# Kernel tuning notes

Hardware: AMD Instinct MI355X
Metric: run time of the kernel (lower is better)

The kernel has to match this reference:

```python
import jax, jax.numpy as jnp
import numpy as np

LN_EPS = 1e-5
NORM_EPS = 1e-12


def channel_layernorm(x, w, b):
    # LayerNorm over channel dim of NCHW tensor (torch permutes to NHWC; equivalent)
    mu = x.mean(axis=1, keepdims=True)
    var = x.var(axis=1, keepdims=True)
    xn = (x - mu) / jnp.sqrt(var + LN_EPS)
    return xn * w[None, :, None, None] + b[None, :, None, None]


def pconv(x, w):
    # 1x1 pointwise conv, w: (out_ch, in_ch)
    return jnp.einsum('bchw,oc->bohw', x, w)


def dwconv3(x, w):
    # depthwise 3x3, padding 1; w: (ch, 1, 3, 3)
    return jax.lax.conv_general_dilated(
        x, w, window_strides=(1, 1), padding='SAME',
        feature_group_count=x.shape[1],
        dimension_numbers=('NCHW', 'OIHW', 'NCHW'))


def l2norm(x):
    n = jnp.sqrt(jnp.sum(x * x, axis=-1, keepdims=True))
    return x / jnp.maximum(n, NORM_EPS)


def setup_inputs() -> dict:
    key = jax.random.key(0)
    ks = jax.random.split(key, 8)
    B, C, H, W = 4, 128, 128, 128
    NH, G = 8, 2

    def w(k, shape, fan_in):
        return jax.random.normal(k, shape, dtype=jnp.float32) * (fan_in ** -0.5)

    return {
        'x': jax.random.normal(ks[0], (B, C, H, W), dtype=jnp.float32),
        'ln1_w': jnp.ones((C,), jnp.float32),
        'ln1_b': jnp.zeros((C,), jnp.float32),
        'temperature': jnp.ones((NH, 1, 1), jnp.float32),
        'qkv_p_w': w(ks[1], (3 * C, C), C),
        'qkv_d_w': w(ks[2], (3 * C, 1, 3, 3), 9),
        'proj_w': w(ks[3], (C, C), C),
        'ln2_w': jnp.ones((C,), jnp.float32),
        'ln2_b': jnp.zeros((C,), jnp.float32),
        'g1_w': w(ks[4], (2 * G * C, C), C),
        'gd_w': w(ks[5], (2 * G * C, 1, 3, 3), 9),
        'g2_w': w(ks[6], (C, G * C), G * C),
        'num_heads': NH,
    }


def reference(x, ln1_w, ln1_b, temperature, qkv_p_w, qkv_d_w, proj_w,
              ln2_w, ln2_b, g1_w, gd_w, g2_w, num_heads):
    b, c, h, w_ = x.shape
    d = c // num_heads

    # --- MDTA branch ---
    y = channel_layernorm(x, ln1_w, ln1_b)
    qkv = dwconv3(pconv(y, qkv_p_w), qkv_d_w)  # (b, 3c, h, w)
    q, k, v = jnp.split(qkv, 3, axis=1)
    q = l2norm(q.reshape(b, num_heads, d, h * w_))
    k = l2norm(k.reshape(b, num_heads, d, h * w_))
    v = v.reshape(b, num_heads, d, h * w_)
    # transposed (channel) attention: (b, heads, d, d)
    attn = jnp.einsum('bhdn,bhen->bhde', q, k) * temperature[None]
    attn = jax.nn.softmax(attn, axis=-1)
    out = jnp.einsum('bhde,bhen->bhdn', attn, v).reshape(b, c, h, w_)
    x = x + pconv(out, proj_w)

    # --- GDFN branch ---
    y = channel_layernorm(x, ln2_w, ln2_b)
    hdn = dwconv3(pconv(y, g1_w), gd_w)  # (b, 2*gamma*c, h, w)
    x1, x2 = jnp.split(hdn, 2, axis=1)
    g = jax.nn.gelu(x1, approximate=False) * x2
    x = x + pconv(g, g2_w)
    return x
```

## Files before the change

### kernel.cpp

```cpp
#include <hip/hip_runtime.h>
#include <cstdint>
#include <cstddef>

typedef float f32x4 __attribute__((ext_vector_type(4)));
typedef __bf16 bf16x8 __attribute__((ext_vector_type(8)));

__device__ __forceinline__ float b2f(unsigned short u) {
    union { unsigned int i; float f; } z; z.i = ((unsigned int)u) << 16; return z.f;
}
__device__ __forceinline__ unsigned short f2b(float f) {
    union { float f; unsigned int i; } z; z.f = f;
    unsigned int x = z.i;
    return (unsigned short)((x + 0x7FFFu + ((x >> 16) & 1u)) >> 16);
}

static constexpr int C = 128;
static constexpr int NP = 16384;
static constexpr int NH = 8;

struct Ptr11 { const float* p[11]; };
__constant__ int kWN[11]   = {128, 128, 8, 49152, 3456, 16384, 128, 128, 65536, 4608, 32768};
__constant__ int kWOff[11] = {0, 128, 256, 272, 49424, 52880, 69264, 69392, 69520, 135056, 139664};
static constexpr int kWTotal = 172432;

__global__ __launch_bounds__(256)
void cvt_w_kernel(Ptr11 P, unsigned short* __restrict__ dst)
{
    int seg = blockIdx.y;
    int n = kWN[seg];
    int i = blockIdx.x * 256 + threadIdx.x;
    if (i >= n) return;
    dst[kWOff[seg] + i] = f2b(P.p[seg][i]);
}

template <int COUT>
__device__ __forceinline__ void gemm_core_tr(
    const unsigned short* BsT,
    const unsigned short* __restrict__ W,
    unsigned short* __restrict__ OutB,
    int n0, int tid)
{
    const int lane = tid & 63;
    const int wid  = tid >> 6;
    const int ln16 = lane & 15, quad = lane >> 4;
    const int wy = wid >> 1, wx = wid & 1;
    const char* bs = (const char*)BsT;
    const int swz = (ln16 & 7) << 4;
    int rbase[4];
    #pragma unroll
    for (int nt = 0; nt < 4; ++nt) {
        int n = wx * 64 + nt * 16 + ln16;
        rbase[nt] = n * 256 + quad * 16;
    }

    for (int cc = 0; cc < COUT / 128; ++cc) {
        const int m0 = cc * 128;
        f32x4 acc[4][4];
        #pragma unroll
        for (int i = 0; i < 4; ++i)
            #pragma unroll
            for (int j = 0; j < 4; ++j) acc[i][j] = f32x4{0.f, 0.f, 0.f, 0.f};

        #pragma unroll
        for (int k0 = 0; k0 < 128; k0 += 32) {
            bf16x8 afr[4], bfr[4];
            #pragma unroll
            for (int mt = 0; mt < 4; ++mt) {
                int m = m0 + wy * 64 + mt * 16 + ln16;
                uint4 v = *(const uint4*)(W + (size_t)m * 128 + k0 + quad * 8);
                afr[mt] = *(bf16x8*)&v;
            }
            #pragma unroll
            for (int nt = 0; nt < 4; ++nt) {
                uint4 v = *(const uint4*)(bs + ((rbase[nt] + k0 * 2) ^ swz));
                bfr[nt] = *(bf16x8*)&v;
            }
            #pragma unroll
            for (int mt = 0; mt < 4; ++mt)
                #pragma unroll
                for (int nt = 0; nt < 4; ++nt)
                    acc[mt][nt] = __builtin_amdgcn_mfma_f32_16x16x32_bf16(
                        afr[mt], bfr[nt], acc[mt][nt], 0, 0, 0);
        }
        #pragma unroll
        for (int mt = 0; mt < 4; ++mt)
            #pragma unroll
            for (int nt = 0; nt < 4; ++nt) {
                int co0 = m0 + wy * 64 + mt * 16 + quad * 4;
                int n = n0 + wx * 64 + nt * 16 + ln16;
                #pragma unroll
                for (int r = 0; r < 4; ++r)
                    OutB[(size_t)(co0 + r) * NP + n] = f2b(acc[mt][nt][r]);
            }
    }
}

template <int COUT>
__global__ __launch_bounds__(256)
void lngemm_kernel(const float* __restrict__ x,
                   const unsigned short* __restrict__ lg,
                   const unsigned short* __restrict__ lb,
                   const unsigned short* __restrict__ W,
                   unsigned short* __restrict__ Out)
{
    __shared__ unsigned short BsT[128 * 128];
    __shared__ float Ssum[8][128], Ssq[8][128], Mu[128], Rs[128];
    const int tid = threadIdx.x;
    const int b = blockIdx.y;
    const int n0 = blockIdx.x * 128;
    const int pxg = tid & 31;
    const int cseg = tid >> 5;
    const float* xb = x + (size_t)b * C * NP + n0 + pxg * 4;

    f32x4 hv[16];
    f32x4 vs = f32x4{0.f, 0.f, 0.f, 0.f}, vq = f32x4{0.f, 0.f, 0.f, 0.f};
    #pragma unroll
    for (int i = 0; i < 16; ++i) {
        f32x4 v = *(const f32x4*)(xb + (size_t)(cseg * 16 + i) * NP);
        hv[i] = v; vs += v; vq += v * v;
    }
    #pragma unroll
    for (int j = 0; j < 4; ++j) {
        Ssum[cseg][pxg * 4 + j] = vs[j];
        Ssq[cseg][pxg * 4 + j]  = vq[j];
    }
    __syncthreads();
    if (tid < 128) {
        float s = 0.f, q = 0.f;
        #pragma unroll
        for (int e = 0; e < 8; ++e) { s += Ssum[e][tid]; q += Ssq[e][tid]; }
        float mu = s * (1.f / 128.f);
        float var = q * (1.f / 128.f) - mu * mu;
        Mu[tid] = mu;
        Rs[tid] = rsqrtf(fmaxf(var, 0.f) + 1e-5f);
    }
    __syncthreads();
    f32x4 mu4 = *(const f32x4*)(&Mu[pxg * 4]);
    f32x4 rs4 = *(const f32x4*)(&Rs[pxg * 4]);

    float gwv[16], bwv[16];
    #pragma unroll
    for (int i = 0; i < 16; ++i) {
        gwv[i] = b2f(lg[cseg * 16 + i]);
        bwv[i] = b2f(lb[cseg * 16 + i]);
    }

    char* p = (char*)BsT;
    #pragma unroll
    for (int j = 0; j < 4; ++j) {
        int n = pxg * 4 + j;
        union { uint4 v[2]; unsigned short u[16]; } o;
        #pragma unroll
        for (int i = 0; i < 16; ++i)
            o.u[i] = f2b((hv[i][j] - mu4[j]) * rs4[j] * gwv[i] + bwv[i]);
        int base = n * 256 + cseg * 32;
        int sw = (n & 7) << 4;
        *(uint4*)(p + (base ^ sw))        = o.v[0];
        *(uint4*)(p + ((base + 16) ^ sw)) = o.v[1];
    }
    __syncthreads();
    gemm_core_tr<COUT>(BsT, W, Out + (size_t)b * COUT * NP, n0, tid);
}

template <int COUT>
__global__ __launch_bounds__(256)
void gemm_bf16t_kernel(const unsigned short* __restrict__ W,
                       const unsigned short* __restrict__ Xt,
                       unsigned short* __restrict__ Out)
{
    __shared__ unsigned short BsT[128 * 128];
    const int tid = threadIdx.x;
    const int b = blockIdx.y;
    const int n0 = blockIdx.x * 128;
    const unsigned short* Xb = Xt + (size_t)b * NP * 128 + (size_t)n0 * 128;
    char* p = (char*)BsT;
    #pragma unroll
    for (int r = 0; r < 8; ++r) {
        int flat = tid + r * 256;
        int n = flat >> 4, ks = flat & 15;
        uint4 v = *(const uint4*)(Xb + (size_t)n * 128 + ks * 8);
        *(uint4*)(p + ((n * 256 + ks * 16) ^ ((n & 7) << 4))) = v;
    }
    __syncthreads();
    gemm_core_tr<COUT>(BsT, W, Out + (size_t)b * COUT * NP, n0, tid);
}

__global__ __launch_bounds__(256)
void projln_kernel(const unsigned short* __restrict__ W,
                   const unsigned short* __restrict__ Yt,
                   const float* __restrict__ Res,
                   float* __restrict__ Xmid,
                   const unsigned short* __restrict__ lg,
                   const unsigned short* __restrict__ lb,
                   unsigned short* __restrict__ Y2t)
{
    __shared__ unsigned short BsT[128 * 128];
    __shared__ float RedS[2][128], RedQ[2][128], Mu[128], Rs[128];
    const int tid = threadIdx.x;
    const int b = blockIdx.y;
    const int n0 = blockIdx.x * 128;
    char* p = (char*)BsT;
    {
        const unsigned short* Xb = Yt + (size_t)b * NP * 128 + (size_t)n0 * 128;
        #pragma unroll
        for (int r = 0; r < 8; ++r) {
            int flat = tid + r * 256;
            int n = flat >> 4, ks = flat & 15;
            uint4 v = *(const uint4*)(Xb + (size_t)n * 128 + ks * 8);
            *(uint4*)(p + ((n * 256 + ks * 16) ^ ((n & 7) << 4))) = v;
        }
    }
    __syncthreads();

    const int lane = tid & 63, wid = tid >> 6;
    const int ln16 = lane & 15, quad = lane >> 4;
    const int wy = wid >> 1, wx = wid & 1;
    const int swz = (ln16 & 7) << 4;
    int rbase[4];
    #pragma unroll
    for (int nt = 0; nt < 4; ++nt) {
        int n = wx * 64 + nt * 16 + ln16;
        rbase[nt] = n * 256 + quad * 16;
    }

    f32x4 acc[4][4];
    #pragma unroll
    for (int i = 0; i < 4; ++i)
        #pragma unroll
        for (int j = 0; j < 4; ++j) acc[i][j] = f32x4{0.f, 0.f, 0.f, 0.f};

    #pragma unroll
    for (int k0 = 0; k0 < 128; k0 += 32) {
        bf16x8 afr[4], bfr[4];
        #pragma unroll
        for (int mt = 0; mt < 4; ++mt) {
            int m = wy * 64 + mt * 16 + ln16;
            uint4 v = *(const uint4*)(W + (size_t)m * 128 + k0 + quad * 8);
            afr[mt] = *(bf16x8*)&v;
        }
        #pragma unroll
        for (int nt = 0; nt < 4; ++nt) {
            uint4 v = *(const uint4*)(p + ((rbase[nt] + k0 * 2) ^ swz));
            bfr[nt] = *(bf16x8*)&v;
        }
        #pragma unroll
        for (int mt = 0; mt < 4; ++mt)
            #pragma unroll
            for (int nt = 0; nt < 4; ++nt)
                acc[mt][nt] = __builtin_amdgcn_mfma_f32_16x16x32_bf16(
                    afr[mt], bfr[nt], acc[mt][nt], 0, 0, 0);
    }

    size_t base = (size_t)b * 128 * NP;
    float ps[4] = {0.f, 0.f, 0.f, 0.f}, pq[4] = {0.f, 0.f, 0.f, 0.f};
    #pragma unroll
    for (int mt = 0; mt < 4; ++mt)
        #pragma unroll
        for (int nt = 0; nt < 4; ++nt) {
            int co0 = wy * 64 + mt * 16 + quad * 4;
            int n = n0 + wx * 64 + nt * 16 + ln16;
            #pragma unroll
            for (int r = 0; r < 4; ++r) {
                size_t idx = base + (size_t)(co0 + r) * NP + n;
                float t = Res[idx] + acc[mt][nt][r];
                Xmid[idx] = t;
                acc[mt][nt][r] = t;
                ps[nt] += t; pq[nt] += t * t;
            }
        }
    #pragma unroll
    for (int nt = 0; nt < 4; ++nt) {
        ps[nt] += __shfl_xor(ps[nt], 16, 64); ps[nt] += __shfl_xor(ps[nt], 32, 64);
        pq[nt] += __shfl_xor(pq[nt], 16, 64); pq[nt] += __shfl_xor(pq[nt], 32, 64);
    }
    if (quad == 0) {
        #pragma unroll
        for (int nt = 0; nt < 4; ++nt) {
            int nn = wx * 64 + nt * 16 + ln16;
            RedS[wy][nn] = ps[nt]; RedQ[wy][nn] = pq[nt];
        }
    }
    __syncthreads();
    if (tid < 128) {
        float s = RedS[0][tid] + RedS[1][tid];
        float q = RedQ[0][tid] + RedQ[1][tid];
        float mu = s * (1.f / 128.f);
        float var = q * (1.f / 128.f) - mu * mu;
        Mu[tid] = mu; Rs[tid] = rsqrtf(fmaxf(var, 0.f) + 1e-5f);
    }
    __syncthreads();

    #pragma unroll
    for (int mt = 0; mt < 4; ++mt) {
        int co0 = wy * 64 + mt * 16 + quad * 4;
        union { uint2 v; unsigned short u[4]; } gv, bv;
        gv.v = *(const uint2*)(lg + co0);
        bv.v = *(const uint2*)(lb + co0);
        float gw[4], bw[4];
        #pragma unroll
        for (int r = 0; r < 4; ++r) { gw[r] = b2f(gv.u[r]); bw[r] = b2f(bv.u[r]); }
        #pragma unroll
        for (int nt = 0; nt < 4; ++nt) {
            int nn = wx * 64 + nt * 16 + ln16;
            float mu = Mu[nn], rs = Rs[nn];
            union { uint2 v; unsigned short u[4]; } t2;
            #pragma unroll
            for (int r = 0; r < 4; ++r)
                t2.u[r] = f2b((acc[mt][nt][r] - mu) * rs * gw[r] + bw[r]);
            int addr = (nn * 256 + co0 * 2) ^ ((nn & 7) << 4);
            *(uint2*)(p + addr) = t2.v;
        }
    }
    __syncthreads();

    unsigned short* Yo = Y2t + (size_t)b * NP * 128 + (size_t)n0 * 128;
    #pragma unroll
    for (int r = 0; r < 8; ++r) {
        int flat = tid + r * 256;
        int n = flat >> 4, ks = flat & 15;
        uint4 v = *(const uint4*)(p + ((n * 256 + ks * 16) ^ ((n & 7) << 4)));
        *(uint4*)(Yo + (size_t)n * 128 + ks * 8) = v;
    }
}

template <int K, int EPI>
__global__ __launch_bounds__(256)
void gemm_pconv(const unsigned short* __restrict__ W,
                const unsigned short* __restrict__ X,
                void* __restrict__ Out,
                const float* __restrict__ Res,
                int Cout)
{
    __shared__ unsigned short Bs[32][130];
    const int tid = threadIdx.x;
    const int b = blockIdx.z;
    const int n0 = blockIdx.x * 128;
    const int m0 = blockIdx.y * 128;
    const unsigned short* Xb = X + (size_t)b * K * NP;
    const int wid = tid >> 6;
    const int lane = tid & 63;
    const int ln16 = lane & 15;
    const int quad = lane >> 4;
    const int wy = wid >> 1;
    const int wx = wid & 1;

    f32x4 acc[4][4];
    #pragma unroll
    for (int i = 0; i < 4; ++i)
        #pragma unroll
        for (int j = 0; j < 4; ++j)
            acc[i][j] = f32x4{0.f, 0.f, 0.f, 0.f};

    for (int k0 = 0; k0 < K; k0 += 32) {
        #pragma unroll
        for (int r = 0; r < 2; ++r) {
            int flat = tid + r * 256;
            int kk = flat >> 4;
            int nn = (flat & 15) * 8;
            uint4 v = *(const uint4*)(Xb + (size_t)(k0 + kk) * NP + n0 + nn);
            unsigned int* d = (unsigned int*)&Bs[kk][nn];
            d[0] = v.x; d[1] = v.y; d[2] = v.z; d[3] = v.w;
        }
        __syncthreads();

        bf16x8 afr[4];
        #pragma unroll
        for (int mt = 0; mt < 4; ++mt) {
            int m = m0 + wy * 64 + mt * 16 + ln16;
            uint4 v = *(const uint4*)(W + (size_t)m * K + k0 + quad * 8);
            afr[mt] = *(bf16x8*)&v;
        }
        bf16x8 bfr[4];
        #pragma unroll
        for (int nt = 0; nt < 4; ++nt) {
            int n = wx * 64 + nt * 16 + ln16;
            union { bf16x8 v; unsigned short u[8]; } tmp;
            #pragma unroll
            for (int j = 0; j < 8; ++j) tmp.u[j] = Bs[quad * 8 + j][n];
            bfr[nt] = tmp.v;
        }
        #pragma unroll
        for (int mt = 0; mt < 4; ++mt)
            #pragma unroll
            for (int nt = 0; nt < 4; ++nt)
                acc[mt][nt] = __builtin_amdgcn_mfma_f32_16x16x32_bf16(
                    afr[mt], bfr[nt], acc[mt][nt], 0, 0, 0);
        __syncthreads();
    }

    size_t outbase = (size_t)b * Cout * NP;
    #pragma unroll
    for (int mt = 0; mt < 4; ++mt) {
        #pragma unroll
        for (int nt = 0; nt < 4; ++nt) {
            int co0 = m0 + wy * 64 + mt * 16 + quad * 4;
            int n = n0 + wx * 64 + nt * 16 + ln16;
            #pragma unroll
            for (int r = 0; r < 4; ++r) {
                float v = acc[mt][nt][r];
                size_t idx = outbase + (size_t)(co0 + r) * NP + n;
                if (EPI == 0) ((unsigned short*)Out)[idx] = f2b(v);
                else          ((float*)Out)[idx] = Res[idx] + v;
            }
        }
    }
}

__global__ __launch_bounds__(256)
void dwconv3_kernel(const unsigned short* __restrict__ in,
                    const unsigned short* __restrict__ w9,
                    unsigned short* __restrict__ out, int CH)
{
    int t = blockIdx.x * 256 + threadIdx.x;
    int xi = (t & 15) * 8;
    int y  = (t >> 4) & 127;
    int bc = t >> 11;
    int c  = bc % CH;
    const unsigned short* base = in + (size_t)bc * NP + y * 128 + xi;

    float wr[9];
    #pragma unroll
    for (int i = 0; i < 9; ++i) wr[i] = b2f(w9[c * 9 + i]);

    uint4 rv0 = uint4{0,0,0,0}, rv1, rv2 = uint4{0,0,0,0};
    if (y > 0)   rv0 = *(const uint4*)(base - 128);
    rv1 = *(const uint4*)(base);
    if (y < 127) rv2 = *(const uint4*)(base + 128);
    uint4 rows[3] = {rv0, rv1, rv2};

    float o[8];
    #pragma unroll
    for (int j = 0; j < 8; ++j) o[j] = 0.f;

    #pragma unroll
    for (int r = 0; r < 3; ++r) {
        union { uint4 v; unsigned short u[8]; } cv; cv.v = rows[r];
        int lh = __shfl_up((int)cv.u[7], 1, 16);
        int rh = __shfl_down((int)cv.u[0], 1, 16);
        float p[10];
        p[0] = (xi > 0)   ? b2f((unsigned short)lh) : 0.f;
        p[9] = (xi < 120) ? b2f((unsigned short)rh) : 0.f;
        #pragma unroll
        for (int j = 0; j < 8; ++j) p[j + 1] = b2f(cv.u[j]);
        #pragma unroll
        for (int j = 0; j < 8; ++j)
            o[j] += wr[r * 3] * p[j] + wr[r * 3 + 1] * p[j + 1] + wr[r * 3 + 2] * p[j + 2];
    }
    union { uint4 v; unsigned short u[8]; } res;
    #pragma unroll
    for (int j = 0; j < 8; ++j) res.u[j] = f2b(o[j]);
    *(uint4*)(out + (size_t)bc * NP + y * 128 + xi) = res.v;
}

__global__ __launch_bounds__(256)
void dwgelu_kernel(const unsigned short* __restrict__ hdn,
                   const unsigned short* __restrict__ w9,
                   unsigned short* __restrict__ g)
{
    int t = blockIdx.x * 256 + threadIdx.x;
    int xi = (t & 15) * 8;
    int y  = (t >> 4) & 127;
    int bc = t >> 11;
    int c  = bc & 255;
    int b  = bc >> 8;
    const unsigned short* base1 = hdn + ((size_t)b * 512 + c) * NP + y * 128 + xi;
    const unsigned short* base2 = base1 + (size_t)256 * NP;

    float w1[9], w2[9];
    #pragma unroll
    for (int i = 0; i < 9; ++i) {
        w1[i] = b2f(w9[c * 9 + i]);
        w2[i] = b2f(w9[(c + 256) * 9 + i]);
    }

    uint4 ra0 = uint4{0,0,0,0}, ra1, ra2 = uint4{0,0,0,0};
    uint4 rb0 = uint4{0,0,0,0}, rb1, rb2 = uint4{0,0,0,0};
    if (y > 0)   { ra0 = *(const uint4*)(base1 - 128); rb0 = *(const uint4*)(base2 - 128); }
    ra1 = *(const uint4*)(base1);
    rb1 = *(const uint4*)(base2);
    if (y < 127) { ra2 = *(const uint4*)(base1 + 128); rb2 = *(const uint4*)(base2 + 128); }
    uint4 rowsA[3] = {ra0, ra1, ra2};
    uint4 rowsB[3] = {rb0, rb1, rb2};

    float a1[8], a2[8];
    #pragma unroll
    for (int j = 0; j < 8; ++j) { a1[j] = 0.f; a2[j] = 0.f; }

    #pragma unroll
    for (int r = 0; r < 3; ++r) {
        union { uint4 v; unsigned short u[8]; } c1, c2;
        c1.v = rowsA[r]; c2.v = rowsB[r];
        int lh1 = __shfl_up((int)c1.u[7], 1, 16);
        int rh1 = __shfl_down((int)c1.u[0], 1, 16);
        int lh2 = __shfl_up((int)c2.u[7], 1, 16);
        int rh2 = __shfl_down((int)c2.u[0], 1, 16);
        float p1[10], p2[10];
        p1[0] = (xi > 0)   ? b2f((unsigned short)lh1) : 0.f;
        p1[9] = (xi < 120) ? b2f((unsigned short)rh1) : 0.f;
        p2[0] = (xi > 0)   ? b2f((unsigned short)lh2) : 0.f;
        p2[9] = (xi < 120) ? b2f((unsigned short)rh2) : 0.f;
        #pragma unroll
        for (int j = 0; j < 8; ++j) { p1[j + 1] = b2f(c1.u[j]); p2[j + 1] = b2f(c2.u[j]); }
        #pragma unroll
        for (int j = 0; j < 8; ++j) {
            a1[j] += w1[r * 3] * p1[j] + w1[r * 3 + 1] * p1[j + 1] + w1[r * 3 + 2] * p1[j + 2];
            a2[j] += w2[r * 3] * p2[j] + w2[r * 3 + 1] * p2[j + 1] + w2[r * 3 + 2] * p2[j + 2];
        }
    }
    union { uint4 v; unsigned short u[8]; } res;
    #pragma unroll
    for (int j = 0; j < 8; ++j) {
        float u = a1[j];
        float tt = u * (0.7978845608f + 0.0356774081f * u * u);
        float e = __expf(2.f * tt);
        float th = 1.f - 2.f / (e + 1.f);
        float ge = 0.5f * u * (1.f + th);
        res.u[j] = f2b(ge * a2[j]);
    }
    *(uint4*)(g + (size_t)bc * NP + y * 128 + xi) = res.v;
}

__global__ __launch_bounds__(256)
void gramss_kernel(const unsigned short* __restrict__ qkv,
                   float* __restrict__ Spart, float* __restrict__ Npart)
{
    int h = blockIdx.x, b = blockIdx.y, sp = blockIdx.z;
    int wid = threadIdx.x >> 6, lane = threadIdx.x & 63;
    int ln16 = lane & 15, quad = lane >> 4;
    int nbase = sp * 2048 + wid * 512;
    const unsigned short* qp = qkv + ((size_t)b * 384 + h * 16 + ln16) * NP;
    const unsigned short* kp = qkv + ((size_t)b * 384 + 128 + h * 16 + ln16) * NP;
    f32x4 acc = f32x4{0.f, 0.f, 0.f, 0.f};
    float qs = 0.f, ks = 0.f;
    for (int i = 0; i < 512; i += 32) {
        int n = nbase + i + quad * 8;
        uint4 av = *(const uint4*)(qp + n);
        uint4 bv = *(const uint4*)(kp + n);
        union { uint4 v; unsigned short u[8]; } ua, ub;
        ua.v = av; ub.v = bv;
        #pragma unroll
        for (int j = 0; j < 8; ++j) {
            float qv = b2f(ua.u[j]); qs += qv * qv;
            float kv = b2f(ub.u[j]); ks += kv * kv;
        }
        acc = __builtin_amdgcn_mfma_f32_16x16x32_bf16(*(bf16x8*)&av, *(bf16x8*)&bv, acc, 0, 0, 0);
    }
    int bh = b * NH + h;
    float* Sp = Spart + ((size_t)bh * 32 + sp * 4 + wid) * 256;
    #pragma unroll
    for (int r = 0; r < 4; ++r)
        Sp[(quad * 4 + r) * 16 + ln16] = acc[r];

    qs += __shfl_xor(qs, 16, 64); qs += __shfl_xor(qs, 32, 64);
    ks += __shfl_xor(ks, 16, 64); ks += __shfl_xor(ks, 32, 64);
    __shared__ float G[4][32];
    if (quad == 0) { G[wid][ln16] = qs; G[wid][16 + ln16] = ks; }
    __syncthreads();
    if (threadIdx.x < 32) {
        float s = G[0][threadIdx.x] + G[1][threadIdx.x] + G[2][threadIdx.x] + G[3][threadIdx.x];
        Npart[((size_t)bh * 8 + sp) * 32 + threadIdx.x] = s;
    }
}

__global__ __launch_bounds__(256)
void softmax2_kernel(const float* __restrict__ Spart, const float* __restrict__ Npart,
                     const unsigned short* __restrict__ temp, float* __restrict__ P)
{
    int bh = blockIdx.x;
    int h = bh & 7;
    int t = threadIdx.x;
    int dq = t >> 4, dk = t & 15;
    float sacc = 0.f;
    const float* Sp = Spart + (size_t)bh * 32 * 256;
    #pragma unroll
    for (int j = 0; j < 32; ++j) sacc += Sp[j * 256 + t];
    const float* Np = Npart + (size_t)bh * 8 * 32;
    float sq = 0.f, sk = 0.f;
    #pragma unroll
    for (int sp = 0; sp < 8; ++sp) { sq += Np[sp * 32 + dq]; sk += Np[sp * 32 + 16 + dk]; }
    float nq = fmaxf(sqrtf(sq), 1e-12f);
    float nk = fmaxf(sqrtf(sk), 1e-12f);
    float v = sacc / (nq * nk) * b2f(temp[h]);
    float m = v;
    #pragma unroll
    for (int o = 8; o > 0; o >>= 1) m = fmaxf(m, __shfl_xor(m, o, 16));
    float e = __expf(v - m);
    float s = e;
    #pragma unroll
    for (int o = 8; o > 0; o >>= 1) s += __shfl_xor(s, o, 16);
    P[(size_t)bh * 256 + t] = e / s;
}

__global__ __launch_bounds__(256)
void attnv_kernel(const float* __restrict__ P, const unsigned short* __restrict__ qkv,
                  unsigned short* __restrict__ yt)
{
    __shared__ float Ps[256];
    int h = blockIdx.y, b = blockIdx.z;
    Ps[threadIdx.x] = P[((size_t)b * NH + h) * 256 + threadIdx.x];
    __syncthreads();
    int n = (blockIdx.x * 256 + threadIdx.x) * 4;
    const unsigned short* vp = qkv + ((size_t)b * 384 + 256 + h * 16) * NP + n;
    float o[16][4];
    #pragma unroll
    for (int d = 0; d < 16; ++d)
        #pragma unroll
        for (int j = 0; j < 4; ++j) o[d][j] = 0.f;
    #pragma unroll
    for (int e = 0; e < 16; ++e) {
        union { uint2 v; unsigned short u[4]; } cv;
        cv.v = *(const uint2*)(vp + (size_t)e * NP);
        float v0 = b2f(cv.u[0]), v1 = b2f(cv.u[1]), v2 = b2f(cv.u[2]), v3 = b2f(cv.u[3]);
        #pragma unroll
        for (int d = 0; d < 16; ++d) {
            float p = Ps[d * 16 + e];
            o[d][0] += p * v0; o[d][1] += p * v1; o[d][2] += p * v2; o[d][3] += p * v3;
        }
    }
    unsigned short* op = yt + (size_t)b * NP * C + (size_t)n * C + h * 16;
    #pragma unroll
    for (int j = 0; j < 4; ++j) {
        union { uint4 v; unsigned short u[8]; } r1, r2;
        #pragma unroll
        for (int d = 0; d < 8; ++d) r1.u[d] = f2b(o[d][j]);
        #pragma unroll
        for (int d = 0; d < 8; ++d) r2.u[d] = f2b(o[8 + d][j]);
        *(uint4*)(op + (size_t)j * C)     = r1.v;
        *(uint4*)(op + (size_t)j * C + 8) = r2.v;
    }
}

struct Bufs {
    float* xmid;
    unsigned short* y;
    unsigned short* y2;
    unsigned short* big;
    unsigned short* mid;
    float* Spart;
    float* P;
    float* Npart;
};

static void run_pipeline(const float* x_f32, float* out_f32,
                         const unsigned short* w,
                         const Bufs& B, int nb, hipStream_t stream)
{
    const unsigned short* ln1_w   = w + 0;
    const unsigned short* ln1_b   = w + 128;
    const unsigned short* temp    = w + 256;
    const unsigned short* qkv_p_w = w + 272;
    const unsigned short* qkv_d_w = w + 49424;
    const unsigned short* proj_w  = w + 52880;
    const unsigned short* ln2_w   = w + 69264;
    const unsigned short* ln2_b   = w + 69392;
    const unsigned short* g1_w    = w + 69520;
    const unsigned short* gd_w    = w + 135056;
    const unsigned short* g2_w    = w + 139664;

    lngemm_kernel<384><<<dim3(NP / 128, nb), 256, 0, stream>>>(x_f32, ln1_w, ln1_b, qkv_p_w, B.big);
    dwconv3_kernel<<<nb * 384 * NP / 2048, 256, 0, stream>>>(B.big, qkv_d_w, B.mid, 384);
    gramss_kernel<<<dim3(NH, nb, 8), 256, 0, stream>>>(B.mid, B.Spart, B.Npart);
    softmax2_kernel<<<nb * NH, 256, 0, stream>>>(B.Spart, B.Npart, temp, B.P);
    attnv_kernel<<<dim3(NP / 1024, NH, nb), 256, 0, stream>>>(B.P, B.mid, B.y);
    projln_kernel<<<dim3(NP / 128, nb), 256, 0, stream>>>(proj_w, B.y, x_f32, B.xmid, ln2_w, ln2_b, B.y2);

    gemm_bf16t_kernel<512><<<dim3(NP / 128, nb), 256, 0, stream>>>(g1_w, B.y2, B.big);
    dwgelu_kernel<<<nb * 256 * NP / 2048, 256, 0, stream>>>(B.big, gd_w, B.mid);
    gemm_pconv<256, 1><<<dim3(NP / 128, 1, nb), 256, 0, stream>>>(g2_w, B.mid, out_f32, B.xmid, 128);
}

extern "C" void kernel_launch(void* const* d_in, const int* in_sizes, int n_in,
                              void* d_out, int out_size, void* d_ws, size_t ws_size,
                              hipStream_t stream)
{
    (void)in_sizes; (void)n_in; (void)out_size;
    const float* x = (const float*)d_in[0];
    char* ws = (char*)d_ws;

    size_t off = 0;
    unsigned short* wpack = (unsigned short*)(ws + off);
    off += (size_t)kWTotal * 2;
    off = (off + 255) & ~(size_t)255;
    size_t header = off;

    auto layout = [&](int nb, size_t o, Bufs& B) -> size_t {
        B.xmid = (float*)(ws + o);           o += (size_t)nb * C * NP * 4;
        B.y    = (unsigned short*)(ws + o);  o += (size_t)nb * C * NP * 2;
        B.y2   = (unsigned short*)(ws + o);  o += (size_t)nb * C * NP * 2;
        B.big  = (unsigned short*)(ws + o);  o += (size_t)nb * 512 * NP * 2;
        B.mid  = (unsigned short*)(ws + o);  o += (size_t)nb * 384 * NP * 2;
        B.Spart = (float*)(ws + o);          o += (size_t)nb * NH * 32 * 256 * 4;
        B.P     = (float*)(ws + o);          o += (size_t)nb * NH * 256 * 4;
        B.Npart = (float*)(ws + o);          o += (size_t)nb * NH * 8 * 32 * 4;
        return o;
    };

    Ptr11 P;
    for (int i = 0; i < 11; ++i) P.p[i] = (const float*)d_in[i + 1];
    cvt_w_kernel<<<dim3(256, 11), 256, 0, stream>>>(P, wpack);

    Bufs Bfull;
    size_t need_full = layout(4, header, Bfull);

    if (ws_size >= need_full) {
        run_pipeline(x, (float*)d_out, wpack, Bfull, 4, stream);
    } else {
        Bufs B1;
        layout(1, header, B1);
        for (int b = 0; b < 4; ++b) {
            run_pipeline(x + (size_t)b * C * NP,
                         (float*)d_out + (size_t)b * C * NP,
                         wpack, B1, 1, stream);
        }
    }
}
```

Measured before the change: 266.7 us.

## Fuse QKV depthwise conv into Gram and attention-V kernels, drop qkv intermediate

The separate depthwise 3x3 conv over the 384 qkv channels is removed. The q/k depthwise conv is now computed inside a new Gram kernel, which stages 4-row tiles in LDS, computes sum-of-squares partials and reduces the per-wave MFMA partials in shared memory. The v depthwise conv is recomputed on the fly inside the attention-V kernel. This avoids writing and re-reading the full bf16 qkv intermediate and saves one launch, at the cost of extra halo loads, redundant row reads, and more partial sums (32 splits) for the softmax kernel to reduce.

```diff
diff --git a/kernel.cpp b/kernel.cpp
--- a/kernel.cpp
+++ b/kernel.cpp
@@ -31,6 +31,32 @@
     int i = blockIdx.x * 256 + threadIdx.x;
     if (i >= n) return;
     dst[kWOff[seg] + i] = f2b(P.p[seg][i]);
+}
+
+__device__ __forceinline__ void dw8(const unsigned short* base, int y, int xi,
+                                    const float* wr, float* o)
+{
+    uint4 rv0 = uint4{0,0,0,0}, rv1, rv2 = uint4{0,0,0,0};
+    if (y > 0)   rv0 = *(const uint4*)(base - 128);
+    rv1 = *(const uint4*)(base);
+    if (y < 127) rv2 = *(const uint4*)(base + 128);
+    uint4 rows[3] = {rv0, rv1, rv2};
+    #pragma unroll
+    for (int j = 0; j < 8; ++j) o[j] = 0.f;
+    #pragma unroll
+    for (int r = 0; r < 3; ++r) {
+        union { uint4 v; unsigned short u[8]; } cv; cv.v = rows[r];
+        int lh = __shfl_up((int)cv.u[7], 1, 16);
+        int rh = __shfl_down((int)cv.u[0], 1, 16);
+        float p[10];
+        p[0] = (xi > 0)   ? b2f((unsigned short)lh) : 0.f;
+        p[9] = (xi < 120) ? b2f((unsigned short)rh) : 0.f;
+        #pragma unroll
+        for (int j = 0; j < 8; ++j) p[j + 1] = b2f(cv.u[j]);
+        #pragma unroll
+        for (int j = 0; j < 8; ++j)
+            o[j] += wr[r * 3] * p[j] + wr[r * 3 + 1] * p[j + 1] + wr[r * 3 + 2] * p[j + 2];
+    }
 }
 
 template <int COUT>
@@ -407,52 +433,6 @@
 }
 
 __global__ __launch_bounds__(256)
-void dwconv3_kernel(const unsigned short* __restrict__ in,
-                    const unsigned short* __restrict__ w9,
-                    unsigned short* __restrict__ out, int CH)
-{
-    int t = blockIdx.x * 256 + threadIdx.x;
-    int xi = (t & 15) * 8;
-    int y  = (t >> 4) & 127;
-    int bc = t >> 11;
-    int c  = bc % CH;
-    const unsigned short* base = in + (size_t)bc * NP + y * 128 + xi;
-
-    float wr[9];
-    #pragma unroll
-    for (int i = 0; i < 9; ++i) wr[i] = b2f(w9[c * 9 + i]);
-
-    uint4 rv0 = uint4{0,0,0,0}, rv1, rv2 = uint4{0,0,0,0};
-    if (y > 0)   rv0 = *(const uint4*)(base - 128);
-    rv1 = *(const uint4*)(base);
-    if (y < 127) rv2 = *(const uint4*)(base + 128);
-    uint4 rows[3] = {rv0, rv1, rv2};
-
-    float o[8];
-    #pragma unroll
-    for (int j = 0; j < 8; ++j) o[j] = 0.f;
-
-    #pragma unroll
-    for (int r = 0; r < 3; ++r) {
-        union { uint4 v; unsigned short u[8]; } cv; cv.v = rows[r];
-        int lh = __shfl_up((int)cv.u[7], 1, 16);
-        int rh = __shfl_down((int)cv.u[0], 1, 16);
-        float p[10];
-        p[0] = (xi > 0)   ? b2f((unsigned short)lh) : 0.f;
-        p[9] = (xi < 120) ? b2f((unsigned short)rh) : 0.f;
-        #pragma unroll
-        for (int j = 0; j < 8; ++j) p[j + 1] = b2f(cv.u[j]);
-        #pragma unroll
-        for (int j = 0; j < 8; ++j)
-            o[j] += wr[r * 3] * p[j] + wr[r * 3 + 1] * p[j + 1] + wr[r * 3 + 2] * p[j + 2];
-    }
-    union { uint4 v; unsigned short u[8]; } res;
-    #pragma unroll
-    for (int j = 0; j < 8; ++j) res.u[j] = f2b(o[j]);
-    *(uint4*)(out + (size_t)bc * NP + y * 128 + xi) = res.v;
-}
-
-__global__ __launch_bounds__(256)
 void dwgelu_kernel(const unsigned short* __restrict__ hdn,
                    const unsigned short* __restrict__ w9,
                    unsigned short* __restrict__ g)
@@ -473,40 +453,10 @@
         w2[i] = b2f(w9[(c + 256) * 9 + i]);
     }
 
-    uint4 ra0 = uint4{0,0,0,0}, ra1, ra2 = uint4{0,0,0,0};
-    uint4 rb0 = uint4{0,0,0,0}, rb1, rb2 = uint4{0,0,0,0};
-    if (y > 0)   { ra0 = *(const uint4*)(base1 - 128); rb0 = *(const uint4*)(base2 - 128); }
-    ra1 = *(const uint4*)(base1);
-    rb1 = *(const uint4*)(base2);
-    if (y < 127) { ra2 = *(const uint4*)(base1 + 128); rb2 = *(const uint4*)(base2 + 128); }
-    uint4 rowsA[3] = {ra0, ra1, ra2};
-    uint4 rowsB[3] = {rb0, rb1, rb2};
-
     float a1[8], a2[8];
-    #pragma unroll
-    for (int j = 0; j < 8; ++j) { a1[j] = 0.f; a2[j] = 0.f; }
-
-    #pragma unroll
-    for (int r = 0; r < 3; ++r) {
-        union { uint4 v; unsigned short u[8]; } c1, c2;
-        c1.v = rowsA[r]; c2.v = rowsB[r];
-        int lh1 = __shfl_up((int)c1.u[7], 1, 16);
-        int rh1 = __shfl_down((int)c1.u[0], 1, 16);
-        int lh2 = __shfl_up((int)c2.u[7], 1, 16);
-        int rh2 = __shfl_down((int)c2.u[0], 1, 16);
-        float p1[10], p2[10];
-        p1[0] = (xi > 0)   ? b2f((unsigned short)lh1) : 0.f;
-        p1[9] = (xi < 120) ? b2f((unsigned short)rh1) : 0.f;
-        p2[0] = (xi > 0)   ? b2f((unsigned short)lh2) : 0.f;
-        p2[9] = (xi < 120) ? b2f((unsigned short)rh2) : 0.f;
-        #pragma unroll
-        for (int j = 0; j < 8; ++j) { p1[j + 1] = b2f(c1.u[j]); p2[j + 1] = b2f(c2.u[j]); }
-        #pragma unroll
-        for (int j = 0; j < 8; ++j) {
-            a1[j] += w1[r * 3] * p1[j] + w1[r * 3 + 1] * p1[j + 1] + w1[r * 3 + 2] * p1[j + 2];
-            a2[j] += w2[r * 3] * p2[j] + w2[r * 3 + 1] * p2[j + 1] + w2[r * 3 + 2] * p2[j + 2];
-        }
-    }
+    dw8(base1, y, xi, w1, a1);
+    dw8(base2, y, xi, w2, a2);
+
     union { uint4 v; unsigned short u[8]; } res;
     #pragma unroll
     for (int j = 0; j < 8; ++j) {
@@ -521,45 +471,66 @@
 }
 
 __global__ __launch_bounds__(256)
-void gramss_kernel(const unsigned short* __restrict__ qkv,
-                   float* __restrict__ Spart, float* __restrict__ Npart)
-{
-    int h = blockIdx.x, b = blockIdx.y, sp = blockIdx.z;
-    int wid = threadIdx.x >> 6, lane = threadIdx.x & 63;
-    int ln16 = lane & 15, quad = lane >> 4;
-    int nbase = sp * 2048 + wid * 512;
-    const unsigned short* qp = qkv + ((size_t)b * 384 + h * 16 + ln16) * NP;
-    const unsigned short* kp = qkv + ((size_t)b * 384 + 128 + h * 16 + ln16) * NP;
+void dwqkgram_kernel(const unsigned short* __restrict__ big,
+                     const unsigned short* __restrict__ w9,
+                     float* __restrict__ Spart,
+                     float* __restrict__ Npart)
+{
+    __shared__ unsigned short qs_[16 * 520];
+    __shared__ unsigned short ks_[16 * 520];
+    __shared__ float Sred[4][256];
+    const int h = blockIdx.x, b = blockIdx.y, sp = blockIdx.z;
+    const int tid = threadIdx.x;
+    const int wid = tid >> 6, lane = tid & 63;
+    const int xi = (tid & 15) * 8;
+    const int yr = (tid >> 4) & 3;
+    const int y  = sp * 4 + yr;
+    const int bh = b * NH + h;
+    float* Np = Npart + ((size_t)bh * 32 + sp) * 32;
+
+    #pragma unroll
+    for (int p = 0; p < 4; ++p) {
+        int qc = p * 4 + wid;
+        #pragma unroll
+        for (int s = 0; s < 2; ++s) {
+            int ch = s * 128 + h * 16 + qc;
+            const unsigned short* base = big + ((size_t)b * 384 + ch) * NP + y * 128 + xi;
+            float wr[9];
+            #pragma unroll
+            for (int i = 0; i < 9; ++i) wr[i] = b2f(w9[ch * 9 + i]);
+            float o[8];
+            dw8(base, y, xi, wr, o);
+            union { uint4 v; unsigned short u[8]; } res;
+            float ss = 0.f;
+            #pragma unroll
+            for (int j = 0; j < 8; ++j) {
+                res.u[j] = f2b(o[j]);
+                float vv = b2f(res.u[j]);
+                ss += vv * vv;
+            }
+            unsigned short* tile = s ? ks_ : qs_;
+            *(uint4*)(&tile[qc * 520 + yr * 128 + xi]) = res.v;
+            #pragma unroll
+            for (int od = 32; od > 0; od >>= 1) ss += __shfl_xor(ss, od, 64);
+            if (lane == 0) Np[s * 16 + qc] = ss;
+        }
+    }
+    __syncthreads();
+
+    const int ln16 = lane & 15, quad = lane >> 4;
     f32x4 acc = f32x4{0.f, 0.f, 0.f, 0.f};
-    float qs = 0.f, ks = 0.f;
-    for (int i = 0; i < 512; i += 32) {
-        int n = nbase + i + quad * 8;
-        uint4 av = *(const uint4*)(qp + n);
-        uint4 bv = *(const uint4*)(kp + n);
-        union { uint4 v; unsigned short u[8]; } ua, ub;
-        ua.v = av; ub.v = bv;
-        #pragma unroll
-        for (int j = 0; j < 8; ++j) {
-            float qv = b2f(ua.u[j]); qs += qv * qv;
-            float kv = b2f(ub.u[j]); ks += kv * kv;
-        }
-        acc = __builtin_amdgcn_mfma_f32_16x16x32_bf16(*(bf16x8*)&av, *(bf16x8*)&bv, acc, 0, 0, 0);
-    }
-    int bh = b * NH + h;
-    float* Sp = Spart + ((size_t)bh * 32 + sp * 4 + wid) * 256;
-    #pragma unroll
-    for (int r = 0; r < 4; ++r)
-        Sp[(quad * 4 + r) * 16 + ln16] = acc[r];
-
-    qs += __shfl_xor(qs, 16, 64); qs += __shfl_xor(qs, 32, 64);
-    ks += __shfl_xor(ks, 16, 64); ks += __shfl_xor(ks, 32, 64);
-    __shared__ float G[4][32];
-    if (quad == 0) { G[wid][ln16] = qs; G[wid][16 + ln16] = ks; }
-    __syncthreads();
-    if (threadIdx.x < 32) {
-        float s = G[0][threadIdx.x] + G[1][threadIdx.x] + G[2][threadIdx.x] + G[3][threadIdx.x];
-        Npart[((size_t)bh * 8 + sp) * 32 + threadIdx.x] = s;
-    }
+    #pragma unroll
+    for (int i = 0; i < 4; ++i) {
+        int off = wid * 128 + i * 32 + quad * 8;
+        uint4 qv = *(const uint4*)(&qs_[ln16 * 520 + off]);
+        uint4 kv = *(const uint4*)(&ks_[ln16 * 520 + off]);
+        acc = __builtin_amdgcn_mfma_f32_16x16x32_bf16(*(bf16x8*)&qv, *(bf16x8*)&kv, acc, 0, 0, 0);
+    }
+    #pragma unroll
+    for (int r = 0; r < 4; ++r) Sred[wid][(quad * 4 + r) * 16 + ln16] = acc[r];
+    __syncthreads();
+    float ssum = Sred[0][tid] + Sred[1][tid] + Sred[2][tid] + Sred[3][tid];
+    Spart[((size_t)bh * 32 + sp) * 256 + tid] = ssum;
 }
 
 __global__ __launch_bounds__(256)
@@ -574,10 +545,10 @@
     const float* Sp = Spart + (size_t)bh * 32 * 256;
     #pragma unroll
     for (int j = 0; j < 32; ++j) sacc += Sp[j * 256 + t];
-    const float* Np = Npart + (size_t)bh * 8 * 32;
+    const float* Np = Npart + (size_t)bh * 32 * 32;
     float sq = 0.f, sk = 0.f;
     #pragma unroll
-    for (int sp = 0; sp < 8; ++sp) { sq += Np[sp * 32 + dq]; sk += Np[sp * 32 + 16 + dk]; }
+    for (int sp = 0; sp < 32; ++sp) { sq += Np[sp * 32 + dq]; sk += Np[sp * 32 + 16 + dk]; }
     float nq = fmaxf(sqrtf(sq), 1e-12f);
     float nk = fmaxf(sqrtf(sk), 1e-12f);
     float v = sacc / (nq * nk) * b2f(temp[h]);
@@ -592,31 +563,60 @@
 }
 
 __global__ __launch_bounds__(256)
-void attnv_kernel(const float* __restrict__ P, const unsigned short* __restrict__ qkv,
-                  unsigned short* __restrict__ yt)
+void attnvdw_kernel(const float* __restrict__ P, const unsigned short* __restrict__ big,
+                    const unsigned short* __restrict__ w9,
+                    unsigned short* __restrict__ yt)
 {
     __shared__ float Ps[256];
     int h = blockIdx.y, b = blockIdx.z;
     Ps[threadIdx.x] = P[((size_t)b * NH + h) * 256 + threadIdx.x];
     __syncthreads();
-    int n = (blockIdx.x * 256 + threadIdx.x) * 4;
-    const unsigned short* vp = qkv + ((size_t)b * 384 + 256 + h * 16) * NP + n;
+    int t = threadIdx.x;
+    int n = (blockIdx.x * 256 + t) * 4;
+    int y  = n >> 7;
+    int x0 = n & 127;
+
     float o[16][4];
     #pragma unroll
     for (int d = 0; d < 16; ++d)
         #pragma unroll
         for (int j = 0; j < 4; ++j) o[d][j] = 0.f;
+
     #pragma unroll
     for (int e = 0; e < 16; ++e) {
-        union { uint2 v; unsigned short u[4]; } cv;
-        cv.v = *(const uint2*)(vp + (size_t)e * NP);
-        float v0 = b2f(cv.u[0]), v1 = b2f(cv.u[1]), v2 = b2f(cv.u[2]), v3 = b2f(cv.u[3]);
+        int ch = 256 + h * 16 + e;
+        const unsigned short* vb = big + ((size_t)b * 384 + ch) * NP + y * 128 + x0;
+        float wr[9];
+        #pragma unroll
+        for (int i = 0; i < 9; ++i) wr[i] = b2f(w9[ch * 9 + i]);
+        uint2 r0 = uint2{0,0}, r1, r2 = uint2{0,0};
+        if (y > 0)   r0 = *(const uint2*)(vb - 128);
+        r1 = *(const uint2*)(vb);
+        if (y < 127) r2 = *(const uint2*)(vb + 128);
+        uint2 rows[3] = {r0, r1, r2};
+        float v4[4] = {0.f, 0.f, 0.f, 0.f};
+        #pragma unroll
+        for (int rr = 0; rr < 3; ++rr) {
+            union { uint2 v; unsigned short u[4]; } cv; cv.v = rows[rr];
+            int lh = __shfl_up((int)cv.u[3], 1, 32);
+            int rh = __shfl_down((int)cv.u[0], 1, 32);
+            float p[6];
+            p[0] = (x0 > 0)   ? b2f((unsigned short)lh) : 0.f;
+            p[5] = (x0 < 124) ? b2f((unsigned short)rh) : 0.f;
+            #pragma unroll
+            for (int j = 0; j < 4; ++j) p[j + 1] = b2f(cv.u[j]);
+            #pragma unroll
+            for (int j = 0; j < 4; ++j)
+                v4[j] += wr[rr * 3] * p[j] + wr[rr * 3 + 1] * p[j + 1] + wr[rr * 3 + 2] * p[j + 2];
+        }
         #pragma unroll
         for (int d = 0; d < 16; ++d) {
-            float p = Ps[d * 16 + e];
-            o[d][0] += p * v0; o[d][1] += p * v1; o[d][2] += p * v2; o[d][3] += p * v3;
-        }
-    }
+            float pw = Ps[d * 16 + e];
+            #pragma unroll
+            for (int j = 0; j < 4; ++j) o[d][j] += pw * v4[j];
+        }
+    }
+
     unsigned short* op = yt + (size_t)b * NP * C + (size_t)n * C + h * 16;
     #pragma unroll
     for (int j = 0; j < 4; ++j) {
@@ -658,10 +658,9 @@
     const unsigned short* g2_w    = w + 139664;
 
     lngemm_kernel<384><<<dim3(NP / 128, nb), 256, 0, stream>>>(x_f32, ln1_w, ln1_b, qkv_p_w, B.big);
-    dwconv3_kernel<<<nb * 384 * NP / 2048, 256, 0, stream>>>(B.big, qkv_d_w, B.mid, 384);
-    gramss_kernel<<<dim3(NH, nb, 8), 256, 0, stream>>>(B.mid, B.Spart, B.Npart);
+    dwqkgram_kernel<<<dim3(NH, nb, 32), 256, 0, stream>>>(B.big, qkv_d_w, B.Spart, B.Npart);
     softmax2_kernel<<<nb * NH, 256, 0, stream>>>(B.Spart, B.Npart, temp, B.P);
-    attnv_kernel<<<dim3(NP / 1024, NH, nb), 256, 0, stream>>>(B.P, B.mid, B.y);
+    attnvdw_kernel<<<dim3(NP / 1024, NH, nb), 256, 0, stream>>>(B.P, B.big, qkv_d_w, B.y);
     projln_kernel<<<dim3(NP / 128, nb), 256, 0, stream>>>(proj_w, B.y, x_f32, B.xmid, ln2_w, ln2_b, B.y2);
 
     gemm_bf16t_kernel<512><<<dim3(NP / 128, nb), 256, 0, stream>>>(g1_w, B.y2, B.big);
@@ -688,10 +687,10 @@
         B.y    = (unsigned short*)(ws + o);  o += (size_t)nb * C * NP * 2;
         B.y2   = (unsigned short*)(ws + o);  o += (size_t)nb * C * NP * 2;
         B.big  = (unsigned short*)(ws + o);  o += (size_t)nb * 512 * NP * 2;
-        B.mid  = (unsigned short*)(ws + o);  o += (size_t)nb * 384 * NP * 2;
+        B.mid  = (unsigned short*)(ws + o);  o += (size_t)nb * 256 * NP * 2;
         B.Spart = (float*)(ws + o);          o += (size_t)nb * NH * 32 * 256 * 4;
         B.P     = (float*)(ws + o);          o += (size_t)nb * NH * 256 * 4;
-        B.Npart = (float*)(ws + o);          o += (size_t)nb * NH * 8 * 32 * 4;
+        B.Npart = (float*)(ws + o);          o += (size_t)nb * NH * 32 * 32 * 4;
         return o;
     };
 
```

Measured after the change: 308.5 us. 1.16x slower.
